# Kernel tuning notes

Hardware: AMD Instinct MI355X
Metric: run time of the kernel (lower is better)

Reference implementation:

```python
import jax, jax.numpy as jnp
import numpy as np
import math

B, S, D, H, L, F, V, C = 8, 1024, 768, 12, 6, 3072, 32000, 10
DK = D // H
EPS = 1e-5


def _pos_encoding(seq_len, d):
    pos = jnp.arange(seq_len, dtype=jnp.float32)[:, None]
    div = jnp.exp(jnp.arange(0, d, 2, dtype=jnp.float32) * (-math.log(10000.0) / d))
    pe = jnp.zeros((seq_len, d), dtype=jnp.float32)
    pe = pe.at[:, 0::2].set(jnp.sin(pos * div))
    pe = pe.at[:, 1::2].set(jnp.cos(pos * div))
    return pe


def _layernorm(x, scale, bias):
    mu = jnp.mean(x, axis=-1, keepdims=True)
    var = jnp.mean(jnp.square(x - mu), axis=-1, keepdims=True)
    return (x - mu) * jax.lax.rsqrt(var + EPS) * scale + bias


def setup_inputs() -> dict:
    key = jax.random.key(0)
    ks = jax.random.split(key, 14)
    s = 0.02
    return {
        "tokens": jax.random.randint(ks[0], (B, S), 0, V),
        "emb": jax.random.normal(ks[1], (V, D), jnp.float32) * s,
        "Wq": jax.random.normal(ks[2], (L, D, D), jnp.float32) * s,
        "Wk": jax.random.normal(ks[3], (L, D, D), jnp.float32) * s,
        "Wv": jax.random.normal(ks[4], (L, D, D), jnp.float32) * s,
        "Wo": jax.random.normal(ks[5], (L, D, D), jnp.float32) * s,
        "W1": jax.random.normal(ks[6], (L, D, F), jnp.float32) * s,
        "W2": jax.random.normal(ks[7], (L, F, D), jnp.float32) * s,
        "ln1_s": jnp.ones((L, D), jnp.float32),
        "ln1_b": jnp.zeros((L, D), jnp.float32),
        "ln2_s": jnp.ones((L, D), jnp.float32),
        "ln2_b": jnp.zeros((L, D), jnp.float32),
        "Wc": jax.random.normal(ks[8], (D, C), jnp.float32) * s,
        "bc": jnp.zeros((C,), jnp.float32),
    }


def _block(x, p):
    Wq, Wk, Wv, Wo, W1, W2, l1s, l1b, l2s, l2b = p
    b, s = x.shape[0], x.shape[1]
    q = (x @ Wq).reshape(b, s, H, DK)
    k = (x @ Wk).reshape(b, s, H, DK)
    v = (x @ Wv).reshape(b, s, H, DK)
    scores = jnp.einsum("bqhd,bkhd->bhqk", q, k) / math.sqrt(DK)
    attn = jax.nn.softmax(scores, axis=-1)
    out = jnp.einsum("bhqk,bkhd->bqhd", attn, v).reshape(b, s, D) @ Wo
    x = _layernorm(x + out, l1s, l1b)
    ffn = jax.nn.relu(x @ W1) @ W2
    x = _layernorm(x + ffn, l2s, l2b)
    return x


def reference(tokens, emb, Wq, Wk, Wv, Wo, W1, W2, ln1_s, ln1_b, ln2_s, ln2_b, Wc, bc):
    x = emb[tokens] + _pos_encoding(tokens.shape[1], D)[None]

    def step(h, p):
        return _block(h, p), None

    x, _ = jax.lax.scan(step, x, (Wq, Wk, Wv, Wo, W1, W2, ln1_s, ln1_b, ln2_s, ln2_b))
    pooled = jnp.mean(x, axis=1)  # [B, D]
    return pooled @ Wc + bc
```

## Files before the change

### kernel.cpp

```cpp
#include <hip/hip_runtime.h>
#include <hip/hip_bf16.h>
#include <math.h>

#define BB 8
#define SS 1024
#define DD 768
#define HH 12
#define LL 6
#define FF 3072
#define CC 10
#define BS_ (BB * SS)

#define WT_STRIDE (2304 * 768 + 768 * 768 + 3072 * 768 + 768 * 3072)

typedef __attribute__((ext_vector_type(8))) short short8v;
typedef __attribute__((ext_vector_type(4))) float f32x4;
typedef __attribute__((ext_vector_type(8))) unsigned short ushort8v;
typedef __attribute__((ext_vector_type(4))) unsigned short ushort4v;
typedef __attribute__((ext_vector_type(2))) unsigned int uint2v;

#define CEXPQ 0.18033688f

__device__ inline unsigned short f2bf(float f) {
  unsigned int u = __builtin_bit_cast(unsigned int, f);
  u += 0x7fffu + ((u >> 16) & 1u);
  return (unsigned short)(u >> 16);
}
__device__ inline float bf2f(unsigned short u) {
  return __builtin_bit_cast(float, (unsigned int)u << 16);
}
__device__ inline unsigned int cvtpk(float lo, float hi) {
  unsigned int r;
  asm("v_cvt_pk_bf16_f32 %0, %1, %2" : "=v"(r) : "v"(lo), "v"(hi));
  return r;
}
__device__ inline void gload16(const void* g, void* l) {
  __builtin_amdgcn_global_load_lds((const __attribute__((address_space(1))) void*)g,
                                   (__attribute__((address_space(3))) void*)l, 16, 0, 0);
}

__device__ inline float wave_sum(float v) {
#pragma unroll
  for (int off = 32; off > 0; off >>= 1) v += __shfl_down(v, off);
  return v;
}

__global__ __launch_bounds__(256) void k_embed(const int* __restrict__ tokens,
                                               const float* __restrict__ emb,
                                               ushort* __restrict__ xb) {
  int row = blockIdx.x;
  int s = row & (SS - 1);
  int tok = tokens[row];
  const float* e = emb + (size_t)tok * DD;
  ushort* xbr = xb + (size_t)row * DD;
  for (int d = threadIdx.x; d < DD; d += 256) {
    float freq = expf((float)(d & ~1) * -0.0119926306f);
    float ang = (float)s * freq;
    float pe = (d & 1) ? cosf(ang) : sinf(ang);
    xbr[d] = f2bf(e[d] + pe);
  }
}

__global__ __launch_bounds__(256) void k_transpose_all(
    const float* __restrict__ Wq, const float* __restrict__ Wk,
    const float* __restrict__ Wv, const float* __restrict__ Wo,
    const float* __restrict__ W1, const float* __restrict__ W2,
    ushort* __restrict__ wt) {
  __shared__ float tile[64][65];
  int bid = blockIdx.x;
  int lyr = blockIdx.y;
  ushort* wqkv_t = wt + (size_t)lyr * WT_STRIDE;
  ushort* wo_t = wqkv_t + 2304 * 768;
  ushort* w1_t = wo_t + 768 * 768;
  ushort* w2_t = w1_t + 3072 * 768;
  const float* W; ushort* Wt; int K, N, lb;
  if (bid < 432) {
    int m = bid / 144; lb = bid - m * 144;
    W = ((m == 0) ? Wq : (m == 1) ? Wk : Wv) + (size_t)lyr * DD * DD;
    Wt = wqkv_t + m * 768 * 768; K = 768; N = 768;
  } else if (bid < 576) {
    W = Wo + (size_t)lyr * DD * DD; Wt = wo_t; K = 768; N = 768; lb = bid - 432;
  } else if (bid < 1152) {
    W = W1 + (size_t)lyr * DD * FF; Wt = w1_t; K = 768; N = 3072; lb = bid - 576;
  } else {
    W = W2 + (size_t)lyr * FF * DD; Wt = w2_t; K = 3072; N = 768; lb = bid - 1152;
  }
  int nbk = K >> 6;
  int k0 = (lb % nbk) * 64, n0 = (lb / nbk) * 64;
  int t = threadIdx.x;
  {
    int r = t >> 2, cl = (t & 3) * 16;
    const float* wrow = W + (size_t)(k0 + r) * N + n0 + cl;
#pragma unroll
    for (int j = 0; j < 4; ++j) {
      float4 v = *(const float4*)(wrow + j * 4);
      tile[r][cl + j * 4 + 0] = v.x; tile[r][cl + j * 4 + 1] = v.y;
      tile[r][cl + j * 4 + 2] = v.z; tile[r][cl + j * 4 + 3] = v.w;
    }
  }
  __syncthreads();
  {
    int n = t >> 2, cq = (t & 3) * 16;
    ushort8v o0, o1;
#pragma unroll
    for (int jj = 0; jj < 8; ++jj) o0[jj] = f2bf(tile[cq + jj][n]);
#pragma unroll
    for (int jj = 0; jj < 8; ++jj) o1[jj] = f2bf(tile[cq + 8 + jj][n]);
    ushort* orow = Wt + (size_t)(n0 + n) * K + k0 + cq;
    *(ushort8v*)(orow) = o0;
    *(ushort8v*)(orow + 8) = o1;
  }
}

template <int RELU, int TN, int SCALEQ = 0>
__global__ __launch_bounds__(256) void k_gemm_db(const ushort* __restrict__ A,
                                                 const ushort* __restrict__ Bt,
                                                 ushort* __restrict__ Cout,
                                                 int M, int N, int K) {
  constexpr int NF = TN / 32;
  __shared__ ushort smem[2][(128 + TN) * 64];
  int bidl = blockIdx.y * gridDim.x + blockIdx.x;
  int nwg = gridDim.x * gridDim.y;
  int cpx = nwg >> 3;
  int tid = (bidl & 7) * cpx + (bidl >> 3);
  int n0 = (tid % gridDim.x) * TN, m0 = (tid / gridDim.x) * 128;
  int t = threadIdx.x, w = t >> 6, l = t & 63;
  int wr = (w >> 1) * 64, wc = (w & 1) * (TN / 2);
  int lr = l & 15, lg = l >> 4;
  f32x4 acc[4][NF] = {};
  int sr8 = l >> 3;
  int scw = ((l & 7) ^ sr8) * 8;
  const ushort* ag = A + (size_t)(m0 + w * 8 + sr8) * K + scw;
  const ushort* bg = Bt + (size_t)(n0 + w * 8 + sr8) * K + scw;
  int nk = K >> 6;

#define STAGE_TILE(KC0, BUF)                                                     \
  {                                                                              \
    ushort* al = &smem[BUF][(w * 8) * 64];                                       \
    ushort* bl = &smem[BUF][128 * 64 + (w * 8) * 64];                            \
    _Pragma("unroll") for (int ii = 0; ii < 4; ++ii)                             \
        gload16(ag + (size_t)ii * 32 * K + (KC0), al + ii * 2048);               \
    _Pragma("unroll") for (int ii = 0; ii < TN / 32; ++ii)                       \
        gload16(bg + (size_t)ii * 32 * K + (KC0), bl + ii * 2048);               \
  }

  STAGE_TILE(0, 0);
  if (nk > 1) STAGE_TILE(64, 1);
  int rsw = lr & 7;
  for (int k = 0; k < nk; ++k) {
    if (k + 1 < nk) {
      if constexpr (TN == 128) asm volatile("s_waitcnt vmcnt(8)" ::: "memory");
      else                     asm volatile("s_waitcnt vmcnt(6)" ::: "memory");
    } else {
      asm volatile("s_waitcnt vmcnt(0)" ::: "memory");
    }
    __builtin_amdgcn_s_barrier();
    __builtin_amdgcn_sched_barrier(0);
    const ushort* As = &smem[k & 1][0];
    const ushort* Bs = &smem[k & 1][128 * 64];
    short8v af[2][4], bfr[2][NF];
#pragma unroll
    for (int ks = 0; ks < 2; ++ks) {
#pragma unroll
      for (int mi = 0; mi < 4; ++mi)
        af[ks][mi] = *(const short8v*)(As + (wr + mi * 16 + lr) * 64 + (((ks * 4 + lg) ^ rsw) << 3));
#pragma unroll
      for (int ni = 0; ni < NF; ++ni)
        bfr[ks][ni] = *(const short8v*)(Bs + (wc + ni * 16 + lr) * 64 + (((ks * 4 + lg) ^ rsw) << 3));
    }
    asm volatile("s_waitcnt lgkmcnt(0)" ::: "memory");
    __builtin_amdgcn_s_barrier();
    __builtin_amdgcn_sched_barrier(0);
    if (k + 2 < nk) STAGE_TILE((k + 2) * 64, k & 1);
    __builtin_amdgcn_s_setprio(1);
#pragma unroll
    for (int ks = 0; ks < 2; ++ks)
#pragma unroll
      for (int mi = 0; mi < 4; ++mi)
#pragma unroll
        for (int ni = 0; ni < NF; ++ni)
          acc[mi][ni] = __builtin_amdgcn_mfma_f32_16x16x32_bf16(af[ks][mi], bfr[ks][ni], acc[mi][ni], 0, 0, 0);
    __builtin_amdgcn_s_setprio(0);
  }
#undef STAGE_TILE
  __syncthreads();
  float osc = (SCALEQ && n0 < 768) ? CEXPQ : 1.0f;
  ushort* cst = &smem[0][0];
#pragma unroll
  for (int mi = 0; mi < 4; ++mi)
#pragma unroll
    for (int ni = 0; ni < NF; ++ni) {
      int cl = wc + ni * 16 + lr;
#pragma unroll
      for (int i = 0; i < 4; ++i) {
        int rl = wr + mi * 16 + lg * 4 + i;
        float v = acc[mi][ni][i];
        if (RELU) v = fmaxf(v, 0.f);
        if (SCALEQ) v *= osc;
        cst[rl * TN + (cl ^ (((rl >> 2) & 3) << 4))] = f2bf(v);
      }
    }
  __syncthreads();
  {
    int row = t >> 1, half = t & 1;
    int swr = ((row >> 2) & 3) << 4;
    ushort* crow = Cout + (size_t)(m0 + row) * N + n0 + half * (TN / 2);
#pragma unroll
    for (int c8 = 0; c8 < TN / 16; ++c8) {
      int c = half * (TN / 2) + c8 * 8;
      ushort8v vv = *(const ushort8v*)(&cst[row * TN + (c ^ swr)]);
      *(ushort8v*)(crow + c8 * 8) = vv;
    }
  }
}

__global__ __launch_bounds__(256) void k_flash(const ushort* __restrict__ qkv,
                                               ushort* __restrict__ ao) {
  __shared__ ushort Ks[64][64];
  __shared__ ushort Vt[64][64];
  __shared__ ushort Ps[4][32][64];
  const int LD = 2304;
  int bidl = blockIdx.y * gridDim.x + blockIdx.x;
  int tid = (bidl & 7) * 96 + (bidl >> 3);
  int qt = tid & 7;
  int bh = tid >> 3;
  int h = bh % HH, b = bh / HH;
  int t = threadIdx.x, w = t >> 6, l = t & 63;
  int lr = l & 15, lg = l >> 4;
  int sw = (l & 7) << 3;
  int q0 = qt * 128;
  const ushort* qbase = qkv + (size_t)(b * SS) * LD + h * 64;
  const ushort* kbase = qbase + 768;
  const ushort* vbase = qbase + 1536;
  short8v qf[2][2];
#pragma unroll
  for (int qg = 0; qg < 2; ++qg) {
    const ushort* qrow = qbase + (size_t)(q0 + w * 32 + qg * 16 + lr) * LD + lg * 8;
    qf[qg][0] = *(const short8v*)(qrow);
    qf[qg][1] = *(const short8v*)(qrow + 32);
  }
  float l_run[2] = {0.f, 0.f};
  f32x4 o_acc[2][4] = {};
  int krow_ = w * 16 + (l >> 3);
  int kcol_ = ((l & 7) * 8) ^ ((krow_ & 7) << 3);
  const ushort* kg = kbase + (size_t)krow_ * LD + kcol_;
  ushort* kl = &Ks[w * 16][0];
  int d_ = t & 7;
  int dk0 = d_ * 8;
  int kv2 = (t >> 3) * 2;
  for (int kt = 0; kt < 16; ++kt) {
    int kv0 = kt * 64;
    const ushort* vr0 = vbase + (size_t)(kv0 + kv2) * LD + dk0;
    ushort8v v0 = *(const ushort8v*)(vr0);
    ushort8v v1 = *(const ushort8v*)(vr0 + LD);
    __syncthreads();
    gload16(kg + (size_t)kv0 * LD, kl);
    gload16(kg + (size_t)(kv0 + 8) * LD, kl + 512);
#pragma unroll
    for (int i = 0; i < 8; ++i) {
      unsigned int pack = (unsigned int)v0[i] | ((unsigned int)v1[i] << 16);
      *(unsigned int*)(&Vt[dk0 + i][kv2 ^ (((i ^ d_) & 7) << 3)]) = pack;
    }
    __syncthreads();
    short8v kf[4][2];
#pragma unroll
    for (int mi = 0; mi < 4; ++mi) {
      int kvr = mi * 16 + lr;
      kf[mi][0] = *(const short8v*)(&Ks[kvr][(lg * 8) ^ sw]);
      kf[mi][1] = *(const short8v*)(&Ks[kvr][(32 + lg * 8) ^ sw]);
    }
    f32x4 s[2][4] = {};
    __builtin_amdgcn_s_setprio(1);
#pragma unroll
    for (int mi = 0; mi < 4; ++mi)
#pragma unroll
      for (int qg = 0; qg < 2; ++qg) {
        s[qg][mi] = __builtin_amdgcn_mfma_f32_16x16x32_bf16(kf[mi][0], qf[qg][0], s[qg][mi], 0, 0, 0);
        s[qg][mi] = __builtin_amdgcn_mfma_f32_16x16x32_bf16(kf[mi][1], qf[qg][1], s[qg][mi], 0, 0, 0);
      }
    __builtin_amdgcn_s_setprio(0);
#pragma unroll
    for (int qg = 0; qg < 2; ++qg) {
      float psum = 0.f;
#pragma unroll
      for (int mi = 0; mi < 4; ++mi) {
        float p0 = exp2f(s[qg][mi][0]);
        float p1 = exp2f(s[qg][mi][1]);
        float p2 = exp2f(s[qg][mi][2]);
        float p3 = exp2f(s[qg][mi][3]);
        psum += (p0 + p1) + (p2 + p3);
        uint2v pp;
        pp.x = cvtpk(p0, p1);
        pp.y = cvtpk(p2, p3);
        *(uint2v*)(&Ps[w][qg * 16 + lr][(mi * 16 + lg * 4) ^ ((lr & 7) << 3)]) = pp;
      }
      psum += __shfl_xor(psum, 16);
      psum += __shfl_xor(psum, 32);
      l_run[qg] += psum;
    }
#pragma unroll
    for (int ks = 0; ks < 2; ++ks) {
      short8v pf[2];
      pf[0] = *(const short8v*)(&Ps[w][lr][(ks * 32 + lg * 8) ^ sw]);
      pf[1] = *(const short8v*)(&Ps[w][16 + lr][(ks * 32 + lg * 8) ^ sw]);
      short8v vf[4];
#pragma unroll
      for (int mi = 0; mi < 4; ++mi) {
        int swz = ((lr & 7) ^ (mi * 2 + (lr >> 3))) & 7;
        vf[mi] = *(const short8v*)(&Vt[mi * 16 + lr][(ks * 32 + lg * 8) ^ (swz << 3)]);
      }
      __builtin_amdgcn_s_setprio(1);
#pragma unroll
      for (int mi = 0; mi < 4; ++mi)
#pragma unroll
        for (int qg = 0; qg < 2; ++qg)
          o_acc[qg][mi] = __builtin_amdgcn_mfma_f32_16x16x32_bf16(vf[mi], pf[qg], o_acc[qg][mi], 0, 0, 0);
      __builtin_amdgcn_s_setprio(0);
    }
  }
#pragma unroll
  for (int qg = 0; qg < 2; ++qg) {
    float invl = 1.f / l_run[qg];
    ushort* orow = ao + (size_t)(b * SS + q0 + w * 32 + qg * 16 + lr) * DD + h * 64;
#pragma unroll
    for (int mi = 0; mi < 4; ++mi) {
      ushort4v o;
#pragma unroll
      for (int i = 0; i < 4; ++i) o[i] = f2bf(o_acc[qg][mi][i] * invl);
      *(ushort4v*)(orow + mi * 16 + lg * 4) = o;
    }
  }
}

__global__ __launch_bounds__(64) void k_addln(ushort* __restrict__ xb,
                                              const ushort* __restrict__ y,
                                              const float* __restrict__ sc,
                                              const float* __restrict__ bi) {
  int row = blockIdx.x, l = threadIdx.x;
  int d0 = l * 12;
  ushort* xr = xb + (size_t)row * DD;
  const ushort* yr = y + (size_t)row * DD;
  ushort4v xa[3], ya[3];
#pragma unroll
  for (int j = 0; j < 3; ++j) {
    xa[j] = *(const ushort4v*)(xr + d0 + j * 4);
    ya[j] = *(const ushort4v*)(yr + d0 + j * 4);
  }
  float v[12];
  float s = 0.f;
#pragma unroll
  for (int j = 0; j < 3; ++j)
#pragma unroll
    for (int i = 0; i < 4; ++i) {
      float vv = bf2f(xa[j][i]) + bf2f(ya[j][i]);
      v[j * 4 + i] = vv;
      s += vv;
    }
  float mu = wave_sum(s);
  mu = __shfl(mu, 0) * (1.f / 768.f);
  float vs = 0.f;
#pragma unroll
  for (int i = 0; i < 12; ++i) {
    float c = v[i] - mu;
    vs += c * c;
  }
  vs = wave_sum(vs);
  float rstd = rsqrtf(__shfl(vs, 0) * (1.f / 768.f) + 1e-5f);
  float4 scv[3], biv[3];
#pragma unroll
  for (int j = 0; j < 3; ++j) {
    scv[j] = *(const float4*)(sc + d0 + j * 4);
    biv[j] = *(const float4*)(bi + d0 + j * 4);
  }
#pragma unroll
  for (int j = 0; j < 3; ++j) {
    ushort4v o;
    const float* sj = (const float*)&scv[j];
    const float* bj = (const float*)&biv[j];
#pragma unroll
    for (int i = 0; i < 4; ++i) o[i] = f2bf((v[j * 4 + i] - mu) * rstd * sj[i] + bj[i]);
    *(ushort4v*)(xr + d0 + j * 4) = o;
  }
}

__global__ __launch_bounds__(256) void k_pool(const ushort* __restrict__ xb,
                                              float* __restrict__ pooled) {
  int b = blockIdx.x, chunk = blockIdx.y, t = threadIdx.x;
  float a0 = 0, a1 = 0, a2 = 0;
  for (int s2 = chunk * 128; s2 < chunk * 128 + 128; ++s2) {
    const ushort* xr = xb + (size_t)(b * SS + s2) * DD;
    a0 += bf2f(xr[t]); a1 += bf2f(xr[t + 256]); a2 += bf2f(xr[t + 512]);
  }
  atomicAdd(&pooled[b * DD + t], a0 * (1.f / 1024.f));
  atomicAdd(&pooled[b * DD + t + 256], a1 * (1.f / 1024.f));
  atomicAdd(&pooled[b * DD + t + 512], a2 * (1.f / 1024.f));
}

__global__ __launch_bounds__(64) void k_cls(const float* __restrict__ pooled,
                                            const float* __restrict__ Wc,
                                            const float* __restrict__ bc,
                                            float* __restrict__ out) {
  int idx = blockIdx.x;
  int b = idx / CC, c = idx % CC;
  int t = threadIdx.x;
  float acc = 0.f;
  for (int d0 = t; d0 < DD; d0 += 64) acc = fmaf(pooled[b * DD + d0], Wc[d0 * CC + c], acc);
  acc = wave_sum(acc);
  if (t == 0) out[b * CC + c] = acc + bc[c];
}

extern "C" void kernel_launch(void* const* d_in, const int* in_sizes, int n_in,
                              void* d_out, int out_size, void* d_ws, size_t ws_size,
                              hipStream_t stream) {
  (void)in_sizes; (void)n_in; (void)out_size; (void)ws_size;
  const int* tokens = (const int*)d_in[0];
  const float* emb = (const float*)d_in[1];
  const float* Wq = (const float*)d_in[2];
  const float* Wk = (const float*)d_in[3];
  const float* Wv = (const float*)d_in[4];
  const float* Wo = (const float*)d_in[5];
  const float* W1 = (const float*)d_in[6];
  const float* W2 = (const float*)d_in[7];
  const float* l1s = (const float*)d_in[8];
  const float* l1b = (const float*)d_in[9];
  const float* l2s = (const float*)d_in[10];
  const float* l2b = (const float*)d_in[11];
  const float* Wc = (const float*)d_in[12];
  const float* bc = (const float*)d_in[13];
  float* out = (float*)d_out;

  char* p = (char*)d_ws;
  ushort* xb = (ushort*)p;              p += (size_t)BS_ * DD * 2;
  ushort* qkvb = (ushort*)p;
  ushort* hb = (ushort*)p;
  ushort* ao = (ushort*)(p + (size_t)BS_ * 2304 * 2);
  p += (size_t)BS_ * FF * 2;
  ushort* yb = (ushort*)p;              p += (size_t)BS_ * DD * 2;
  ushort* wt = (ushort*)p;              p += (size_t)WT_STRIDE * LL * 2;
  float* pooled = (float*)p;

  k_embed<<<BS_, 256, 0, stream>>>(tokens, emb, xb);
  k_transpose_all<<<dim3(1728, LL), 256, 0, stream>>>(Wq, Wk, Wv, Wo, W1, W2, wt);

  for (int l = 0; l < LL; ++l) {
    ushort* wqkv_t = wt + (size_t)l * WT_STRIDE;
    ushort* wo_t = wqkv_t + 2304 * 768;
    ushort* w1_t = wo_t + 768 * 768;
    ushort* w2_t = w1_t + 3072 * 768;

    k_gemm_db<0, 128, 1><<<dim3(2304 / 128, BS_ / 128), 256, 0, stream>>>(xb, wqkv_t, qkvb, BS_, 2304, DD);
    k_flash<<<dim3(8, BB * HH), 256, 0, stream>>>(qkvb, ao);
    k_gemm_db<0, 64><<<dim3(DD / 64, BS_ / 128), 256, 0, stream>>>(ao, wo_t, yb, BS_, DD, DD);
    k_addln<<<BS_, 64, 0, stream>>>(xb, yb, l1s + l * DD, l1b + l * DD);
    k_gemm_db<1, 128><<<dim3(FF / 128, BS_ / 128), 256, 0, stream>>>(xb, w1_t, hb, BS_, FF, DD);
    k_gemm_db<0, 64><<<dim3(DD / 64, BS_ / 128), 256, 0, stream>>>(hb, w2_t, yb, BS_, DD, FF);
    k_addln<<<BS_, 64, 0, stream>>>(xb, yb, l2s + l * DD, l2b + l * DD);
  }

  hipMemsetAsync(pooled, 0, (size_t)BB * DD * sizeof(float), stream);
  k_pool<<<dim3(BB, 8), 256, 0, stream>>>(xb, pooled);
  k_cls<<<BB * CC, 64, 0, stream>>>(pooled, Wc, bc, out);
}
```

Before: 1.399 ms.

## Double-buffer K and V tiles in flash attention to overlap loads with compute

Turns the K and transposed-V shared-memory tiles into double buffers. Before the loop a prologue loads the first tile; inside the loop each iteration issues the next tile's async K load and V register loads before computing on the current buffer. The next V tile is transposed into LDS at the end of the iteration, so there is one barrier per iteration instead of two. This hides global-load latency but doubles K/V LDS usage and holds prefetched V values in registers, which may lower occupancy.

Result: slower. 1.489 ms (+6.4%).

```diff
diff --git a/kernel.cpp b/kernel.cpp
--- a/kernel.cpp
+++ b/kernel.cpp
@@ -216,8 +216,8 @@
 
 __global__ __launch_bounds__(256) void k_flash(const ushort* __restrict__ qkv,
                                                ushort* __restrict__ ao) {
-  __shared__ ushort Ks[64][64];
-  __shared__ ushort Vt[64][64];
+  __shared__ ushort Ks[2][64][64];
+  __shared__ ushort Vt[2][64][64];
   __shared__ ushort Ps[4][32][64];
   const int LD = 2304;
   int bidl = blockIdx.y * gridDim.x + blockIdx.x;
@@ -244,30 +244,38 @@
   int krow_ = w * 16 + (l >> 3);
   int kcol_ = ((l & 7) * 8) ^ ((krow_ & 7) << 3);
   const ushort* kg = kbase + (size_t)krow_ * LD + kcol_;
-  ushort* kl = &Ks[w * 16][0];
   int d_ = t & 7;
   int dk0 = d_ * 8;
   int kv2 = (t >> 3) * 2;
-  for (int kt = 0; kt < 16; ++kt) {
-    int kv0 = kt * 64;
-    const ushort* vr0 = vbase + (size_t)(kv0 + kv2) * LD + dk0;
-    ushort8v v0 = *(const ushort8v*)(vr0);
-    ushort8v v1 = *(const ushort8v*)(vr0 + LD);
-    __syncthreads();
-    gload16(kg + (size_t)kv0 * LD, kl);
-    gload16(kg + (size_t)(kv0 + 8) * LD, kl + 512);
+  const ushort* vg = vbase + (size_t)kv2 * LD + dk0;
+  {
+    gload16(kg, &Ks[0][w * 16][0]);
+    gload16(kg + (size_t)8 * LD, &Ks[0][w * 16 + 8][0]);
+    ushort8v v0 = *(const ushort8v*)(vg);
+    ushort8v v1 = *(const ushort8v*)(vg + LD);
 #pragma unroll
     for (int i = 0; i < 8; ++i) {
       unsigned int pack = (unsigned int)v0[i] | ((unsigned int)v1[i] << 16);
-      *(unsigned int*)(&Vt[dk0 + i][kv2 ^ (((i ^ d_) & 7) << 3)]) = pack;
+      *(unsigned int*)(&Vt[0][dk0 + i][kv2 ^ (((i ^ d_) & 7) << 3)]) = pack;
     }
     __syncthreads();
+  }
+  for (int kt = 0; kt < 16; ++kt) {
+    int cur = kt & 1, nxt = cur ^ 1;
+    ushort8v v0n, v1n;
+    if (kt < 15) {
+      size_t off = (size_t)(kt + 1) * 64 * LD;
+      gload16(kg + off, &Ks[nxt][w * 16][0]);
+      gload16(kg + off + (size_t)8 * LD, &Ks[nxt][w * 16 + 8][0]);
+      v0n = *(const ushort8v*)(vg + off);
+      v1n = *(const ushort8v*)(vg + off + LD);
+    }
     short8v kf[4][2];
 #pragma unroll
     for (int mi = 0; mi < 4; ++mi) {
       int kvr = mi * 16 + lr;
-      kf[mi][0] = *(const short8v*)(&Ks[kvr][(lg * 8) ^ sw]);
-      kf[mi][1] = *(const short8v*)(&Ks[kvr][(32 + lg * 8) ^ sw]);
+      kf[mi][0] = *(const short8v*)(&Ks[cur][kvr][(lg * 8) ^ sw]);
+      kf[mi][1] = *(const short8v*)(&Ks[cur][kvr][(32 + lg * 8) ^ sw]);
     }
     f32x4 s[2][4] = {};
     __builtin_amdgcn_s_setprio(1);
@@ -307,7 +315,7 @@
 #pragma unroll
       for (int mi = 0; mi < 4; ++mi) {
         int swz = ((lr & 7) ^ (mi * 2 + (lr >> 3))) & 7;
-        vf[mi] = *(const short8v*)(&Vt[mi * 16 + lr][(ks * 32 + lg * 8) ^ (swz << 3)]);
+        vf[mi] = *(const short8v*)(&Vt[cur][mi * 16 + lr][(ks * 32 + lg * 8) ^ (swz << 3)]);
       }
       __builtin_amdgcn_s_setprio(1);
 #pragma unroll
@@ -317,6 +325,14 @@
           o_acc[qg][mi] = __builtin_amdgcn_mfma_f32_16x16x32_bf16(vf[mi], pf[qg], o_acc[qg][mi], 0, 0, 0);
       __builtin_amdgcn_s_setprio(0);
     }
+    if (kt < 15) {
+#pragma unroll
+      for (int i = 0; i < 8; ++i) {
+        unsigned int pack = (unsigned int)v0n[i] | ((unsigned int)v1n[i] << 16);
+        *(unsigned int*)(&Vt[nxt][dk0 + i][kv2 ^ (((i ^ d_) & 7) << 3)]) = pack;
+      }
+    }
+    __syncthreads();
   }
 #pragma unroll
   for (int qg = 0; qg < 2; ++qg) {
```
